# Performance work log

Hardware: AMD Instinct MI355X
Metric: run time of the kernel (lower is better)

Reference implementation:

```python
import jax, jax.numpy as jnp
import numpy as np

B, H, W, F, D = 8, 126, 126, 64, 32
ITERS, NIT = 3, 20
RHO, NU, DT, FRC = 1.0, 0.1, 0.1, 1.0
DX = 2.0 / (B + 1)
DY = 2.0 / (H + 1)
DX2, DY2 = DX * DX, DY * DY
DEN = 2.0 * (DX2 + DY2)


def _b_term(du_dx, dv_dy, du_dy, dv_dx):
    return RHO * ((du_dx + dv_dy) / DT - du_dx**2 - 2.0 * du_dy * dv_dx - dv_dy**2)


def build_b(u, v):
    b = jnp.zeros_like(u)
    # interior
    b = b.at[:, 1:-1, 1:-1].set(_b_term(
        (u[:, 1:-1, 2:] - u[:, 1:-1, :-2]) / (2 * DX),
        (v[:, 2:, 1:-1] - v[:, :-2, 1:-1]) / (2 * DY),
        (u[:, 2:, 1:-1] - u[:, :-2, 1:-1]) / (2 * DY),
        (v[:, 1:-1, 2:] - v[:, 1:-1, :-2]) / (2 * DX)))
    # periodic wrap, last column
    b = b.at[:, 1:-1, -1].set(_b_term(
        (u[:, 1:-1, 0] - u[:, 1:-1, -2]) / (2 * DX),
        (v[:, 2:, -1] - v[:, :-2, -1]) / (2 * DY),
        (u[:, 2:, -1] - u[:, :-2, -1]) / (2 * DY),
        (v[:, 1:-1, 0] - v[:, 1:-1, -2]) / (2 * DX)))
    # periodic wrap, first column
    b = b.at[:, 1:-1, 0].set(_b_term(
        (u[:, 1:-1, 1] - u[:, 1:-1, -1]) / (2 * DX),
        (v[:, 2:, 0] - v[:, :-2, 0]) / (2 * DY),
        (u[:, 2:, 0] - u[:, :-2, 0]) / (2 * DY),
        (v[:, 1:-1, 1] - v[:, 1:-1, -1]) / (2 * DX)))
    return b


def pressure_poisson(p, b):
    c = DX2 * DY2 / DEN

    def step(p, _):
        pn = p
        p = p.at[:, 1:-1, 1:-1].set(
            ((pn[:, 1:-1, 2:] + pn[:, 1:-1, :-2]) * DY2 + (pn[:, 2:, 1:-1] + pn[:, :-2, 1:-1]) * DX2) / DEN
            - c * b[:, 1:-1, 1:-1])
        p = p.at[:, 1:-1, -1].set(
            ((pn[:, 1:-1, 0] + pn[:, 1:-1, -2]) * DY2 + (pn[:, 2:, -1] + pn[:, :-2, -1]) * DX2) / DEN
            - c * b[:, 1:-1, -1])
        p = p.at[:, 1:-1, 0].set(
            ((pn[:, 1:-1, 1] + pn[:, 1:-1, -1]) * DY2 + (pn[:, 2:, 0] + pn[:, :-2, 0]) * DX2) / DEN
            - c * b[:, 1:-1, 0])
        # Neumann-style row boundaries (copy from updated p, as in torch code)
        p = p.at[:, -1].set(p[:, -2])
        p = p.at[:, 0].set(p[:, 1])
        return p, None

    p, _ = jax.lax.scan(step, p, None, length=NIT)
    return p


def velocity_step(u, v, p):
    un, vn = u, v
    uc = un[:, 1:-1, 1:-1]
    vc = vn[:, 1:-1, 1:-1]
    u_i = (uc - uc * DT / DX * (uc - un[:, 1:-1, :-2]) - vc * DT / DY * (uc - un[:, :-2, 1:-1])
           - DT / (2 * RHO * DX) * (p[:, 1:-1, 2:] - p[:, 1:-1, :-2])
           + NU * (DT / DX2 * (un[:, 1:-1, 2:] - 2 * uc + un[:, 1:-1, :-2])
                   + DT / DY2 * (un[:, 2:, 1:-1] - 2 * uc + un[:, :-2, 1:-1]))
           + FRC * DT)
    v_i = (vc - uc * DT / DX * (vc - vn[:, 1:-1, :-2]) - vc * DT / DY * (vc - vn[:, :-2, 1:-1])
           - DT / (2 * RHO * DY) * (p[:, 2:, 1:-1] - p[:, :-2, 1:-1])
           + NU * (DT / DX2 * (vn[:, 1:-1, 2:] - 2 * vc + vn[:, 1:-1, :-2])
                   + DT / DY2 * (vn[:, 2:, 1:-1] - 2 * vc + vn[:, :-2, 1:-1])))
    ue = un[:, 1:-1, -1]
    ve = vn[:, 1:-1, -1]
    u_e = (ue - ue * DT / DX * (ue - un[:, 1:-1, -2]) - ve * DT / DY * (ue - un[:, :-2, -1])
           - DT / (2 * RHO * DX) * (p[:, 1:-1, 0] - p[:, 1:-1, -2])
           + NU * (DT / DX2 * (un[:, 1:-1, 0] - 2 * ue + un[:, 1:-1, -2])
                   + DT / DY2 * (un[:, 2:, -1] - 2 * ue + un[:, :-2, -1]))
           + FRC * DT)
    v_e = (ve - ue * DT / DX * (ve - vn[:, 1:-1, -2]) - ve * DT / DY * (ve - vn[:, :-2, -1])
           - DT / (2 * RHO * DY) * (p[:, 2:, -1] - p[:, :-2, -1])
           + NU * (DT / DX2 * (vn[:, 1:-1, 0] - 2 * ve + vn[:, 1:-1, -2])
                   + DT / DY2 * (vn[:, 2:, -1] - 2 * ve + vn[:, :-2, -1])))
    u0c = un[:, 1:-1, 0]
    v0c = vn[:, 1:-1, 0]
    u_0 = (u0c - u0c * DT / DX * (u0c - un[:, 1:-1, -1]) - v0c * DT / DY * (u0c - un[:, :-2, 0])
           - DT / (2 * RHO * DX) * (p[:, 1:-1, 1] - p[:, 1:-1, -1])
           + NU * (DT / DX2 * (un[:, 1:-1, 1] - 2 * u0c + un[:, 1:-1, -1])
                   + DT / DY2 * (un[:, 2:, 0] - 2 * u0c + un[:, :-2, 0]))
           + FRC * DT)
    v_0 = (v0c - u0c * DT / DX * (v0c - vn[:, 1:-1, -1]) - v0c * DT / DY * (v0c - vn[:, :-2, 0])
           - DT / (2 * RHO * DY) * (p[:, 2:, 0] - p[:, :-2, 0])
           + NU * (DT / DX2 * (vn[:, 1:-1, 1] - 2 * v0c + vn[:, 1:-1, -1])
                   + DT / DY2 * (vn[:, 2:, 0] - 2 * v0c + vn[:, :-2, 0])))
    u = un.at[:, 1:-1, 1:-1].set(u_i).at[:, 1:-1, -1].set(u_e).at[:, 1:-1, 0].set(u_0)
    v = vn.at[:, 1:-1, 1:-1].set(v_i).at[:, 1:-1, -1].set(v_e).at[:, 1:-1, 0].set(v_0)
    u = u.at[:, 0].set(0.0).at[:, -1].set(0.0)
    v = v.at[:, 0].set(0.0).at[:, -1].set(0.0)
    return u, v


def setup_inputs() -> dict:
    key = jax.random.key(0)
    ks = jax.random.split(key, 5)
    x = jax.random.normal(ks[0], (B, H, W, F), jnp.float32) * 0.05
    u0 = jax.random.normal(ks[1], (B, H + 2, W + 2, D), jnp.float32) * 0.05
    v0 = jax.random.normal(ks[2], (B, H + 2, W + 2, D), jnp.float32) * 0.05
    w = jax.random.normal(ks[3], (D, F), jnp.float32) / np.float32(np.sqrt(F))
    b_lin = jax.random.normal(ks[4], (D,), jnp.float32) * 0.01
    return {"x": x, "u0": u0, "v0": v0, "w": w, "b_lin": b_lin}


def reference(x, u0, v0, w, b_lin):
    # pad spatial dims by 1 then linear preprocess: (B,H+2,W+2,F) -> (B,H+2,W+2,D)
    p = jnp.pad(x, ((0, 0), (1, 1), (1, 1), (0, 0)))
    p = jnp.einsum('bhwf,df->bhwd', p, w) + b_lin
    u, v = u0, v0
    for _ in range(ITERS):
        b = build_b(u, v)
        p = pressure_poisson(p, b)
        u, v = velocity_step(u, v, p)
    return p[:, -1, :, :]  # (B, W+2, D)
```

## Files before the change

### kernel.cpp

```cpp
#include <hip/hip_runtime.h>

#define NITER 20
#define OUTER 3

constexpr double DXd  = 2.0 / 9.0;
constexpr double DYd  = 2.0 / 127.0;
constexpr double DX2d = DXd * DXd;
constexpr double DY2d = DYd * DYd;
constexpr double DENd = 2.0 * (DX2d + DY2d);

constexpr float K1     = (float)(DY2d / DENd);
constexpr float K2     = (float)(DX2d / DENd);
constexpr float CC     = (float)(DX2d * DY2d / DENd);
constexpr float INV2DX = (float)(1.0 / (2.0 * DXd));
constexpr float INV2DY = (float)(1.0 / (2.0 * DYd));
constexpr float INVDT  = (float)(1.0 / 0.1);
constexpr float DTDX   = (float)(0.1 / DXd);
constexpr float DTDY   = (float)(0.1 / DYd);
constexpr float PGX    = (float)(0.1 / (2.0 * 1.0 * DXd));
constexpr float PGY    = (float)(0.1 / (2.0 * 1.0 * DYd));
constexpr float A1     = (float)(0.1 / DX2d);
constexpr float A2     = (float)(0.1 / DY2d);
constexpr float NUf    = 0.1f;
constexpr float FDT    = 0.1f;

__device__ __forceinline__ float bperm(int srcByte, float v) {
    return __int_as_float(__builtin_amdgcn_ds_bpermute(srcByte, __float_as_int(v)));
}

__global__ __launch_bounds__(256) void einsum_kernel(
    const float* __restrict__ x, const float* __restrict__ w,
    const float* __restrict__ bl, float* __restrict__ p0)
{
    int id = blockIdx.x * 256 + threadIdx.x;
    int c = id & 127, r = (id >> 7) & 127, b = id >> 14;
    float acc[32];
#pragma unroll
    for (int d = 0; d < 32; ++d) acc[d] = bl[d];
    if (r >= 1 && r <= 126 && c >= 1 && c <= 126) {
        const float* xp = x + (((size_t)(b * 126 + (r - 1))) * 126 + (c - 1)) * 64;
#pragma unroll
        for (int f = 0; f < 64; f += 4) {
            float4 xv = *(const float4*)(xp + f);
#pragma unroll
            for (int d = 0; d < 32; ++d) {
                acc[d] += xv.x * w[d * 64 + f] + xv.y * w[d * 64 + f + 1]
                        + xv.z * w[d * 64 + f + 2] + xv.w * w[d * 64 + f + 3];
            }
        }
    }
    float* op = p0 + ((size_t)b * 32) * 16384 + r * 128 + c;
#pragma unroll
    for (int d = 0; d < 32; ++d) op[(size_t)d * 16384] = acc[d];
}

__global__ __launch_bounds__(512, 2) void sim_kernel(
    const float* __restrict__ u0, const float* __restrict__ v0,
    const float* __restrict__ p0ws, const float* __restrict__ x,
    const float* __restrict__ w, const float* __restrict__ bl,
    float* __restrict__ out, int use_ws)
{
    __shared__ float sP[2][16][2][128];
    __shared__ float sU[16][2][128];
    __shared__ float sV[16][2][128];

    const int tid = threadIdx.x;
    const int tx = tid & 31, ty = tid >> 5;
    const int c0 = tx << 2, r0 = ty << 3;
    const int lane = tid & 63;
    const int srcL = (((lane & 32) | ((lane + 31) & 31)) << 2);
    const int srcR = (((lane & 32) | ((lane + 1) & 31)) << 2);
    const int bb = blockIdx.x & 7;
    const int d  = blockIdx.x >> 3;

    float pC[8][4], uC[8][4], vC[8][4], cb[8][4];

#pragma unroll
    for (int r = 0; r < 8; ++r) {
        const size_t base = ((size_t)((bb * 128 + (r0 + r)) * 128 + c0)) * 32 + d;
#pragma unroll
        for (int c = 0; c < 4; ++c) {
            uC[r][c] = u0[base + (size_t)c * 32];
            vC[r][c] = v0[base + (size_t)c * 32];
        }
    }

    if (use_ws) {
        const float* pp = p0ws + ((size_t)(bb * 32 + d)) * 16384;
#pragma unroll
        for (int r = 0; r < 8; ++r) {
            float4 t = *(const float4*)(pp + (r0 + r) * 128 + c0);
            pC[r][0] = t.x; pC[r][1] = t.y; pC[r][2] = t.z; pC[r][3] = t.w;
        }
    } else {
        const float blv = bl[d];
#pragma unroll
        for (int r = 0; r < 8; ++r) {
            const int gr = r0 + r;
#pragma unroll
            for (int c = 0; c < 4; ++c) {
                const int gc = c0 + c;
                float acc = blv;
                if (gr >= 1 && gr <= 126 && gc >= 1 && gc <= 126) {
                    const float* xp = x + (((size_t)(bb * 126 + (gr - 1))) * 126 + (gc - 1)) * 64;
                    for (int f = 0; f < 64; f += 4) {
                        float4 xv = *(const float4*)(xp + f);
                        acc += xv.x * w[d * 64 + f] + xv.y * w[d * 64 + f + 1]
                             + xv.z * w[d * 64 + f + 2] + xv.w * w[d * 64 + f + 3];
                    }
                }
                pC[r][c] = acc;
            }
        }
    }

    int s = 0;
    *(float4*)&sP[0][ty][0][c0] = make_float4(pC[0][0], pC[0][1], pC[0][2], pC[0][3]);
    *(float4*)&sP[0][ty][1][c0] = make_float4(pC[7][0], pC[7][1], pC[7][2], pC[7][3]);
    *(float4*)&sU[ty][0][c0]    = make_float4(uC[0][0], uC[0][1], uC[0][2], uC[0][3]);
    *(float4*)&sU[ty][1][c0]    = make_float4(uC[7][0], uC[7][1], uC[7][2], uC[7][3]);
    *(float4*)&sV[ty][0][c0]    = make_float4(vC[0][0], vC[0][1], vC[0][2], vC[0][3]);
    *(float4*)&sV[ty][1][c0]    = make_float4(vC[7][0], vC[7][1], vC[7][2], vC[7][3]);
    __syncthreads();

    const int tyN = (ty > 0) ? ty - 1 : 0;
    const int tyS = (ty < 15) ? ty + 1 : 15;

    for (int outer = 0; outer < OUTER; ++outer) {
        {
            float4 uN4 = *(const float4*)&sU[tyN][1][c0];
            float4 uS4 = *(const float4*)&sU[tyS][0][c0];
            float4 vN4 = *(const float4*)&sV[tyN][1][c0];
            float4 vS4 = *(const float4*)&sV[tyS][0][c0];
            float uNh[4] = {uN4.x, uN4.y, uN4.z, uN4.w};
            float uSh[4] = {uS4.x, uS4.y, uS4.z, uS4.w};
            float vNh[4] = {vN4.x, vN4.y, vN4.z, vN4.w};
            float vSh[4] = {vS4.x, vS4.y, vS4.z, vS4.w};
#pragma unroll
            for (int r = 0; r < 8; ++r) {
                float uWh = bperm(srcL, uC[r][3]);
                float uEh = bperm(srcR, uC[r][0]);
                float vWh = bperm(srcL, vC[r][3]);
                float vEh = bperm(srcR, vC[r][0]);
#pragma unroll
                for (int c = 0; c < 4; ++c) {
                    float uE = (c < 3) ? uC[r][c + 1] : uEh;
                    float uW = (c > 0) ? uC[r][c - 1] : uWh;
                    float vE = (c < 3) ? vC[r][c + 1] : vEh;
                    float vW = (c > 0) ? vC[r][c - 1] : vWh;
                    float uN = (r > 0) ? uC[r - 1][c] : uNh[c];
                    float uS = (r < 7) ? uC[r + 1][c] : uSh[c];
                    float vN = (r > 0) ? vC[r - 1][c] : vNh[c];
                    float vS = (r < 7) ? vC[r + 1][c] : vSh[c];
                    float dudx = (uE - uW) * INV2DX;
                    float dvdy = (vS - vN) * INV2DY;
                    float dudy = (uS - uN) * INV2DY;
                    float dvdx = (vE - vW) * INV2DX;
                    float bt = (dudx + dvdy) * INVDT - dudx * dudx
                             - 2.0f * dudy * dvdx - dvdy * dvdy;
                    cb[r][c] = CC * bt;
                }
            }
        }

        for (int it = 0; it < NITER; ++it) {
            float4 t4 = *(const float4*)&sP[s][tyN][1][c0];
            float4 b4 = *(const float4*)&sP[s][tyS][0][c0];
            float nrow[4] = {t4.x, t4.y, t4.z, t4.w};
            float shalo[4] = {b4.x, b4.y, b4.z, b4.w};
#pragma unroll
            for (int r = 0; r < 8; ++r) {
                float old0[4];
#pragma unroll
                for (int c = 0; c < 4; ++c) old0[c] = pC[r][c];
                float pWh = bperm(srcL, old0[3]);
                float pEh = bperm(srcR, old0[0]);
#pragma unroll
                for (int c = 0; c < 4; ++c) {
                    float E = (c < 3) ? old0[c + 1] : pEh;
                    float W = (c > 0) ? old0[c - 1] : pWh;
                    float N = nrow[c];
                    float S = (r < 7) ? pC[r + 1][c] : shalo[c];
                    pC[r][c] = (E + W) * K1 + (N + S) * K2 - cb[r][c];
                }
#pragma unroll
                for (int c = 0; c < 4; ++c) nrow[c] = old0[c];
            }
            if (ty == 0) {
#pragma unroll
                for (int c = 0; c < 4; ++c) pC[0][c] = pC[1][c];
            }
            if (ty == 15) {
#pragma unroll
                for (int c = 0; c < 4; ++c) pC[7][c] = pC[6][c];
            }
            *(float4*)&sP[s ^ 1][ty][0][c0] = make_float4(pC[0][0], pC[0][1], pC[0][2], pC[0][3]);
            *(float4*)&sP[s ^ 1][ty][1][c0] = make_float4(pC[7][0], pC[7][1], pC[7][2], pC[7][3]);
            __syncthreads();
            s ^= 1;
        }

        if (outer < OUTER - 1) {
            float4 ut4 = *(const float4*)&sU[tyN][1][c0];
            float4 us4 = *(const float4*)&sU[tyS][0][c0];
            float4 vt4 = *(const float4*)&sV[tyN][1][c0];
            float4 vs4 = *(const float4*)&sV[tyS][0][c0];
            float4 pt4 = *(const float4*)&sP[s][tyN][1][c0];
            float4 pb4 = *(const float4*)&sP[s][tyS][0][c0];
            float uNh[4] = {ut4.x, ut4.y, ut4.z, ut4.w};
            float uSh[4] = {us4.x, us4.y, us4.z, us4.w};
            float vNh[4] = {vt4.x, vt4.y, vt4.z, vt4.w};
            float vSh[4] = {vs4.x, vs4.y, vs4.z, vs4.w};
            float pNh[4] = {pt4.x, pt4.y, pt4.z, pt4.w};
            float pSh[4] = {pb4.x, pb4.y, pb4.z, pb4.w};
            __syncthreads();

            float uNrow[4], vNrow[4];
#pragma unroll
            for (int c = 0; c < 4; ++c) { uNrow[c] = uNh[c]; vNrow[c] = vNh[c]; }
#pragma unroll
            for (int r = 0; r < 8; ++r) {
                float uold[4], vold[4];
#pragma unroll
                for (int c = 0; c < 4; ++c) { uold[c] = uC[r][c]; vold[c] = vC[r][c]; }
                float uWh = bperm(srcL, uold[3]);
                float uEh = bperm(srcR, uold[0]);
                float vWh = bperm(srcL, vold[3]);
                float vEh = bperm(srcR, vold[0]);
                float pWh = bperm(srcL, pC[r][3]);
                float pEh = bperm(srcR, pC[r][0]);
#pragma unroll
                for (int c = 0; c < 4; ++c) {
                    float uc = uold[c], vc = vold[c];
                    float uE = (c < 3) ? uold[c + 1] : uEh;
                    float uW = (c > 0) ? uold[c - 1] : uWh;
                    float vE = (c < 3) ? vold[c + 1] : vEh;
                    float vW = (c > 0) ? vold[c - 1] : vWh;
                    float uN = uNrow[c];
                    float uS = (r < 7) ? uC[r + 1][c] : uSh[c];
                    float vN = vNrow[c];
                    float vS = (r < 7) ? vC[r + 1][c] : vSh[c];
                    float pE = (c < 3) ? pC[r][c + 1] : pEh;
                    float pW = (c > 0) ? pC[r][c - 1] : pWh;
                    float pN = (r > 0) ? pC[r - 1][c] : pNh[c];
                    float pS = (r < 7) ? pC[r + 1][c] : pSh[c];

                    float unew = uc - uc * DTDX * (uc - uW) - vc * DTDY * (uc - uN)
                               - PGX * (pE - pW)
                               + NUf * (A1 * (uE - 2.0f * uc + uW) + A2 * (uS - 2.0f * uc + uN))
                               + FDT;
                    float vnew = vc - uc * DTDX * (vc - vW) - vc * DTDY * (vc - vN)
                               - PGY * (pS - pN)
                               + NUf * (A1 * (vE - 2.0f * vc + vW) + A2 * (vS - 2.0f * vc + vN));
                    uC[r][c] = unew;
                    vC[r][c] = vnew;
                }
#pragma unroll
                for (int c = 0; c < 4; ++c) { uNrow[c] = uold[c]; vNrow[c] = vold[c]; }
            }
            if (ty == 0) {
#pragma unroll
                for (int c = 0; c < 4; ++c) { uC[0][c] = 0.0f; vC[0][c] = 0.0f; }
            }
            if (ty == 15) {
#pragma unroll
                for (int c = 0; c < 4; ++c) { uC[7][c] = 0.0f; vC[7][c] = 0.0f; }
            }
            *(float4*)&sU[ty][0][c0] = make_float4(uC[0][0], uC[0][1], uC[0][2], uC[0][3]);
            *(float4*)&sU[ty][1][c0] = make_float4(uC[7][0], uC[7][1], uC[7][2], uC[7][3]);
            *(float4*)&sV[ty][0][c0] = make_float4(vC[0][0], vC[0][1], vC[0][2], vC[0][3]);
            *(float4*)&sV[ty][1][c0] = make_float4(vC[7][0], vC[7][1], vC[7][2], vC[7][3]);
            __syncthreads();
        }
    }

    if (ty == 15) {
        float* op = out + ((size_t)bb * 128 + c0) * 32 + d;
        op[0]  = pC[7][0];
        op[32] = pC[7][1];
        op[64] = pC[7][2];
        op[96] = pC[7][3];
    }
}

extern "C" void kernel_launch(void* const* d_in, const int* in_sizes, int n_in,
                              void* d_out, int out_size, void* d_ws, size_t ws_size,
                              hipStream_t stream) {
    const float* x  = (const float*)d_in[0];
    const float* u0 = (const float*)d_in[1];
    const float* v0 = (const float*)d_in[2];
    const float* w  = (const float*)d_in[3];
    const float* bl = (const float*)d_in[4];
    float* out = (float*)d_out;
    float* p0  = (float*)d_ws;

    const size_t need = (size_t)8 * 32 * 128 * 128 * sizeof(float);
    const int use_ws = (ws_size >= need) ? 1 : 0;

    if (use_ws) {
        einsum_kernel<<<512, 256, 0, stream>>>(x, w, bl, p0);
    }
    sim_kernel<<<256, 512, 0, stream>>>(u0, v0, p0, x, w, bl, out, use_ws);
}
```

Baseline: 246.8 us.

## Fuse two Jacobi sweeps per barrier using two-row halos and shared-memory source term

```diff
diff --git a/kernel.cpp b/kernel.cpp
--- a/kernel.cpp
+++ b/kernel.cpp
@@ -60,9 +60,8 @@
     const float* __restrict__ w, const float* __restrict__ bl,
     float* __restrict__ out, int use_ws)
 {
-    __shared__ float sP[2][16][2][128];
-    __shared__ float sU[16][2][128];
-    __shared__ float sV[16][2][128];
+    __shared__ float sP[2][16][4][128];
+    __shared__ float sCB[16][8][128];
 
     const int tid = threadIdx.x;
     const int tx = tid & 31, ty = tid >> 5;
@@ -73,7 +72,7 @@
     const int bb = blockIdx.x & 7;
     const int d  = blockIdx.x >> 3;
 
-    float pC[8][4], uC[8][4], vC[8][4], cb[8][4];
+    float pC[8][4], uC[8][4], vC[8][4];
 
 #pragma unroll
     for (int r = 0; r < 8; ++r) {
@@ -114,24 +113,25 @@
         }
     }
 
-    int s = 0;
-    *(float4*)&sP[0][ty][0][c0] = make_float4(pC[0][0], pC[0][1], pC[0][2], pC[0][3]);
-    *(float4*)&sP[0][ty][1][c0] = make_float4(pC[7][0], pC[7][1], pC[7][2], pC[7][3]);
-    *(float4*)&sU[ty][0][c0]    = make_float4(uC[0][0], uC[0][1], uC[0][2], uC[0][3]);
-    *(float4*)&sU[ty][1][c0]    = make_float4(uC[7][0], uC[7][1], uC[7][2], uC[7][3]);
-    *(float4*)&sV[ty][0][c0]    = make_float4(vC[0][0], vC[0][1], vC[0][2], vC[0][3]);
-    *(float4*)&sV[ty][1][c0]    = make_float4(vC[7][0], vC[7][1], vC[7][2], vC[7][3]);
-    __syncthreads();
-
     const int tyN = (ty > 0) ? ty - 1 : 0;
     const int tyS = (ty < 15) ? ty + 1 : 15;
 
+    *(float4*)&sP[0][ty][0][c0] = make_float4(pC[0][0], pC[0][1], pC[0][2], pC[0][3]);
+    *(float4*)&sP[0][ty][1][c0] = make_float4(pC[1][0], pC[1][1], pC[1][2], pC[1][3]);
+    *(float4*)&sP[0][ty][2][c0] = make_float4(pC[6][0], pC[6][1], pC[6][2], pC[6][3]);
+    *(float4*)&sP[0][ty][3][c0] = make_float4(pC[7][0], pC[7][1], pC[7][2], pC[7][3]);
+    *(float4*)&sP[1][ty][0][c0] = make_float4(uC[0][0], uC[0][1], uC[0][2], uC[0][3]);
+    *(float4*)&sP[1][ty][1][c0] = make_float4(uC[7][0], uC[7][1], uC[7][2], uC[7][3]);
+    *(float4*)&sP[1][ty][2][c0] = make_float4(vC[0][0], vC[0][1], vC[0][2], vC[0][3]);
+    *(float4*)&sP[1][ty][3][c0] = make_float4(vC[7][0], vC[7][1], vC[7][2], vC[7][3]);
+    __syncthreads();
+
     for (int outer = 0; outer < OUTER; ++outer) {
         {
-            float4 uN4 = *(const float4*)&sU[tyN][1][c0];
-            float4 uS4 = *(const float4*)&sU[tyS][0][c0];
-            float4 vN4 = *(const float4*)&sV[tyN][1][c0];
-            float4 vS4 = *(const float4*)&sV[tyS][0][c0];
+            float4 uN4 = *(const float4*)&sP[1][tyN][1][c0];
+            float4 uS4 = *(const float4*)&sP[1][tyS][0][c0];
+            float4 vN4 = *(const float4*)&sP[1][tyN][3][c0];
+            float4 vS4 = *(const float4*)&sP[1][tyS][2][c0];
             float uNh[4] = {uN4.x, uN4.y, uN4.z, uN4.w};
             float uSh[4] = {uS4.x, uS4.y, uS4.z, uS4.w};
             float vNh[4] = {vN4.x, vN4.y, vN4.z, vN4.w};
@@ -142,6 +142,7 @@
                 float uEh = bperm(srcR, uC[r][0]);
                 float vWh = bperm(srcL, vC[r][3]);
                 float vEh = bperm(srcR, vC[r][0]);
+                float cbr[4];
 #pragma unroll
                 for (int c = 0; c < 4; ++c) {
                     float uE = (c < 3) ? uC[r][c + 1] : uEh;
@@ -158,33 +159,96 @@
                     float dvdx = (vE - vW) * INV2DX;
                     float bt = (dudx + dvdy) * INVDT - dudx * dudx
                              - 2.0f * dudy * dvdx - dvdy * dvdy;
-                    cb[r][c] = CC * bt;
-                }
-            }
-        }
-
-        for (int it = 0; it < NITER; ++it) {
-            float4 t4 = *(const float4*)&sP[s][tyN][1][c0];
-            float4 b4 = *(const float4*)&sP[s][tyS][0][c0];
-            float nrow[4] = {t4.x, t4.y, t4.z, t4.w};
-            float shalo[4] = {b4.x, b4.y, b4.z, b4.w};
+                    cbr[c] = CC * bt;
+                }
+                *(float4*)&sCB[ty][r][c0] = make_float4(cbr[0], cbr[1], cbr[2], cbr[3]);
+            }
+        }
+        __syncthreads();
+
+        for (int ph = 0; ph < NITER / 2; ++ph) {
+            const int rs = ph & 1;
+            float4 om1 = *(const float4*)&sP[rs][tyN][3][c0];
+            float  om1W = sP[rs][tyN][3][(c0 + 127) & 127];
+            float  om1E = sP[rs][tyN][3][(c0 + 4) & 127];
+            float4 om2 = *(const float4*)&sP[rs][tyN][2][c0];
+            float4 op8 = *(const float4*)&sP[rs][tyS][0][c0];
+            float  op8W = sP[rs][tyS][0][(c0 + 127) & 127];
+            float  op8E = sP[rs][tyS][0][(c0 + 4) & 127];
+            float4 op9 = *(const float4*)&sP[rs][tyS][1][c0];
+            float4 cbm1 = *(const float4*)&sCB[tyN][7][c0];
+            float4 cbp8 = *(const float4*)&sCB[tyS][0][c0];
+
+            float am[4], ac[4], ap[4], cbCur[4];
+            {
+                float o0 = om1W, o1 = om1.x, o2 = om1.y, o3 = om1.z, o4 = om1.w, o5 = om1E;
+                am[0] = (o2 + o0) * K1 + (om2.x + pC[0][0]) * K2 - cbm1.x;
+                am[1] = (o3 + o1) * K1 + (om2.y + pC[0][1]) * K2 - cbm1.y;
+                am[2] = (o4 + o2) * K1 + (om2.z + pC[0][2]) * K2 - cbm1.z;
+                am[3] = (o5 + o3) * K1 + (om2.w + pC[0][3]) * K2 - cbm1.w;
+            }
+            {
+                float W = bperm(srcL, pC[0][3]);
+                float E = bperm(srcR, pC[0][0]);
+                float4 cb0 = *(const float4*)&sCB[ty][0][c0];
+                cbCur[0] = cb0.x; cbCur[1] = cb0.y; cbCur[2] = cb0.z; cbCur[3] = cb0.w;
+                float om1a[4] = {om1.x, om1.y, om1.z, om1.w};
+#pragma unroll
+                for (int c = 0; c < 4; ++c) {
+                    float E_ = (c < 3) ? pC[0][c + 1] : E;
+                    float W_ = (c > 0) ? pC[0][c - 1] : W;
+                    ac[c] = (E_ + W_) * K1 + (om1a[c] + pC[1][c]) * K2 - cbCur[c];
+                }
+            }
 #pragma unroll
             for (int r = 0; r < 8; ++r) {
-                float old0[4];
-#pragma unroll
-                for (int c = 0; c < 4; ++c) old0[c] = pC[r][c];
-                float pWh = bperm(srcL, old0[3]);
-                float pEh = bperm(srcR, old0[0]);
-#pragma unroll
-                for (int c = 0; c < 4; ++c) {
-                    float E = (c < 3) ? old0[c + 1] : pEh;
-                    float W = (c > 0) ? old0[c - 1] : pWh;
-                    float N = nrow[c];
-                    float S = (r < 7) ? pC[r + 1][c] : shalo[c];
-                    pC[r][c] = (E + W) * K1 + (N + S) * K2 - cb[r][c];
-                }
-#pragma unroll
-                for (int c = 0; c < 4; ++c) nrow[c] = old0[c];
+                float cbN[4];
+                if (r < 7) {
+                    float W = bperm(srcL, pC[r + 1][3]);
+                    float E = bperm(srcR, pC[r + 1][0]);
+                    float4 cbv = *(const float4*)&sCB[ty][r + 1][c0];
+                    cbN[0] = cbv.x; cbN[1] = cbv.y; cbN[2] = cbv.z; cbN[3] = cbv.w;
+                    float Sr[4];
+                    if (r + 1 < 7) {
+#pragma unroll
+                        for (int c = 0; c < 4; ++c) Sr[c] = pC[r + 2][c];
+                    } else {
+                        Sr[0] = op8.x; Sr[1] = op8.y; Sr[2] = op8.z; Sr[3] = op8.w;
+                    }
+#pragma unroll
+                    for (int c = 0; c < 4; ++c) {
+                        float E_ = (c < 3) ? pC[r + 1][c + 1] : E;
+                        float W_ = (c > 0) ? pC[r + 1][c - 1] : W;
+                        ap[c] = (E_ + W_) * K1 + (pC[r][c] + Sr[c]) * K2 - cbN[c];
+                    }
+                } else {
+                    float o0 = op8W, o1 = op8.x, o2 = op8.y, o3 = op8.z, o4 = op8.w, o5 = op8E;
+                    cbN[0] = cbp8.x; cbN[1] = cbp8.y; cbN[2] = cbp8.z; cbN[3] = cbp8.w;
+                    ap[0] = (o2 + o0) * K1 + (pC[7][0] + op9.x) * K2 - cbN[0];
+                    ap[1] = (o3 + o1) * K1 + (pC[7][1] + op9.y) * K2 - cbN[1];
+                    ap[2] = (o4 + o2) * K1 + (pC[7][2] + op9.z) * K2 - cbN[2];
+                    ap[3] = (o5 + o3) * K1 + (pC[7][3] + op9.w) * K2 - cbN[3];
+                }
+                if (r == 0 && ty == 0) {
+#pragma unroll
+                    for (int c = 0; c < 4; ++c) ac[c] = ap[c];
+                }
+                if (r == 6 && ty == 15) {
+#pragma unroll
+                    for (int c = 0; c < 4; ++c) ap[c] = ac[c];
+                }
+                {
+                    float W = bperm(srcL, ac[3]);
+                    float E = bperm(srcR, ac[0]);
+#pragma unroll
+                    for (int c = 0; c < 4; ++c) {
+                        float E_ = (c < 3) ? ac[c + 1] : E;
+                        float W_ = (c > 0) ? ac[c - 1] : W;
+                        pC[r][c] = (E_ + W_) * K1 + (am[c] + ap[c]) * K2 - cbCur[c];
+                    }
+                }
+#pragma unroll
+                for (int c = 0; c < 4; ++c) { am[c] = ac[c]; ac[c] = ap[c]; cbCur[c] = cbN[c]; }
             }
             if (ty == 0) {
 #pragma unroll
@@ -194,19 +258,26 @@
 #pragma unroll
                 for (int c = 0; c < 4; ++c) pC[7][c] = pC[6][c];
             }
-            *(float4*)&sP[s ^ 1][ty][0][c0] = make_float4(pC[0][0], pC[0][1], pC[0][2], pC[0][3]);
-            *(float4*)&sP[s ^ 1][ty][1][c0] = make_float4(pC[7][0], pC[7][1], pC[7][2], pC[7][3]);
+            *(float4*)&sP[rs ^ 1][ty][0][c0] = make_float4(pC[0][0], pC[0][1], pC[0][2], pC[0][3]);
+            *(float4*)&sP[rs ^ 1][ty][1][c0] = make_float4(pC[1][0], pC[1][1], pC[1][2], pC[1][3]);
+            *(float4*)&sP[rs ^ 1][ty][2][c0] = make_float4(pC[6][0], pC[6][1], pC[6][2], pC[6][3]);
+            *(float4*)&sP[rs ^ 1][ty][3][c0] = make_float4(pC[7][0], pC[7][1], pC[7][2], pC[7][3]);
             __syncthreads();
-            s ^= 1;
         }
 
         if (outer < OUTER - 1) {
-            float4 ut4 = *(const float4*)&sU[tyN][1][c0];
-            float4 us4 = *(const float4*)&sU[tyS][0][c0];
-            float4 vt4 = *(const float4*)&sV[tyN][1][c0];
-            float4 vs4 = *(const float4*)&sV[tyS][0][c0];
-            float4 pt4 = *(const float4*)&sP[s][tyN][1][c0];
-            float4 pb4 = *(const float4*)&sP[s][tyS][0][c0];
+            *(float4*)&sP[1][ty][0][c0] = make_float4(uC[0][0], uC[0][1], uC[0][2], uC[0][3]);
+            *(float4*)&sP[1][ty][1][c0] = make_float4(uC[7][0], uC[7][1], uC[7][2], uC[7][3]);
+            *(float4*)&sP[1][ty][2][c0] = make_float4(vC[0][0], vC[0][1], vC[0][2], vC[0][3]);
+            *(float4*)&sP[1][ty][3][c0] = make_float4(vC[7][0], vC[7][1], vC[7][2], vC[7][3]);
+            __syncthreads();
+
+            float4 ut4 = *(const float4*)&sP[1][tyN][1][c0];
+            float4 us4 = *(const float4*)&sP[1][tyS][0][c0];
+            float4 vt4 = *(const float4*)&sP[1][tyN][3][c0];
+            float4 vs4 = *(const float4*)&sP[1][tyS][2][c0];
+            float4 pt4 = *(const float4*)&sP[0][tyN][3][c0];
+            float4 pb4 = *(const float4*)&sP[0][tyS][0][c0];
             float uNh[4] = {ut4.x, ut4.y, ut4.z, ut4.w};
             float uSh[4] = {us4.x, us4.y, us4.z, us4.w};
             float vNh[4] = {vt4.x, vt4.y, vt4.z, vt4.w};
@@ -266,10 +337,10 @@
 #pragma unroll
                 for (int c = 0; c < 4; ++c) { uC[7][c] = 0.0f; vC[7][c] = 0.0f; }
             }
-            *(float4*)&sU[ty][0][c0] = make_float4(uC[0][0], uC[0][1], uC[0][2], uC[0][3]);
-            *(float4*)&sU[ty][1][c0] = make_float4(uC[7][0], uC[7][1], uC[7][2], uC[7][3]);
-            *(float4*)&sV[ty][0][c0] = make_float4(vC[0][0], vC[0][1], vC[0][2], vC[0][3]);
-            *(float4*)&sV[ty][1][c0] = make_float4(vC[7][0], vC[7][1], vC[7][2], vC[7][3]);
+            *(float4*)&sP[1][ty][0][c0] = make_float4(uC[0][0], uC[0][1], uC[0][2], uC[0][3]);
+            *(float4*)&sP[1][ty][1][c0] = make_float4(uC[7][0], uC[7][1], uC[7][2], uC[7][3]);
+            *(float4*)&sP[1][ty][2][c0] = make_float4(vC[0][0], vC[0][1], vC[0][2], vC[0][3]);
+            *(float4*)&sP[1][ty][3][c0] = make_float4(vC[7][0], vC[7][1], vC[7][2], vC[7][3]);
             __syncthreads();
         }
     }
```

After: 251.5 us. About the same (+1.9%).
